# Kernel optimization log

Measured on AMD Instinct MI355X. Metric: run time of the kernel, lower is better.

Reference implementation:

```python
import jax, jax.numpy as jnp
import numpy as np

N = 50000       # nodes
E = 800000      # raw edges (self-loops added in reference, per PyG GATConv default)
F_IN = 256      # input feature dim (dataset.num_features stand-in)
H = 4           # heads (layer 1)
C = 32          # hidden_channels per head
CLS = 16        # num_classes (layer 2 out, heads=1)


def setup_inputs() -> dict:
    key = jax.random.key(0)
    ks = jax.random.split(key, 12)
    s = 0.05
    return {
        "x": jax.random.normal(ks[0], (N, F_IN), jnp.float32),
        "edge_index": jax.random.randint(ks[1], (2, E), 0, N, dtype=jnp.int64),
        "W1": jax.random.normal(ks[2], (F_IN, H * C), jnp.float32) * s,
        "att_src1": jax.random.normal(ks[3], (H, C), jnp.float32) * s,
        "att_dst1": jax.random.normal(ks[4], (H, C), jnp.float32) * s,
        "b1": jnp.zeros((H * C,), jnp.float32),
        "W2": jax.random.normal(ks[5], (H * C, CLS), jnp.float32) * s,
        "att_src2": jax.random.normal(ks[6], (1, CLS), jnp.float32) * s,
        "att_dst2": jax.random.normal(ks[7], (1, CLS), jnp.float32) * s,
        "b2": jnp.zeros((CLS,), jnp.float32),
    }


def gat_conv(x, src, dst, W, a_src, a_dst, b, heads, ch):
    """One GATConv (concat=True). src/dst include self-loops."""
    n = x.shape[0]
    h = (x @ W).reshape(n, heads, ch)                       # [N,H,C]
    alpha_s = jnp.sum(h * a_src, axis=-1)                   # [N,H]
    alpha_d = jnp.sum(h * a_dst, axis=-1)                   # [N,H]
    e = jax.nn.leaky_relu(alpha_s[src] + alpha_d[dst], 0.2) # [E',H]
    # segment softmax over incoming edges of each destination node
    m = jax.ops.segment_max(e, dst, num_segments=n)         # [N,H]
    ex = jnp.exp(e - m[dst])
    den = jax.ops.segment_sum(ex, dst, num_segments=n)      # [N,H]
    coef = ex / (den[dst] + 1e-16)                          # [E',H]
    # weighted scatter-aggregate of source features
    out = jax.ops.segment_sum(h[src] * coef[:, :, None], dst, num_segments=n)
    return out.reshape(n, heads * ch) + b


def reference(x, edge_index, W1, att_src1, att_dst1, b1, W2, att_src2, att_dst2, b2):
    n = x.shape[0]
    loop = jnp.arange(n, dtype=edge_index.dtype)
    src = jnp.concatenate([edge_index[0], loop])
    dst = jnp.concatenate([edge_index[1], loop])
    # eval mode: F.dropout is identity
    h = gat_conv(x, src, dst, W1, att_src1, att_dst1, b1, H, C)
    h = jax.nn.elu(h)
    out = gat_conv(h, src, dst, W2, att_src2, att_dst2, b2, 1, CLS)
    return out
```

## Files before the change

kernel.cpp:

```cpp
#include <hip/hip_runtime.h>
#include <hip/hip_bf16.h>
#include <math.h>

#define NNODES 50000
#define FIN 256
#define HH 4
#define CC 32
#define D1 128
#define CLS 16
#define NBUCK ((NNODES + 255) >> 8)
#define CHUNK 4096
#define GEMMBLK ((NNODES + 63) / 64)
#define WPREPBLK ((FIN*D1 + 255) / 256)

typedef __attribute__((ext_vector_type(8))) short bfrag8;
typedef __attribute__((ext_vector_type(4))) float facc4;

__device__ __forceinline__ float lrelu(float x){ return x > 0.f ? x : 0.2f*x; }

__device__ __forceinline__ float fexp(float x){
#if __has_builtin(__builtin_amdgcn_exp2f)
  return __builtin_amdgcn_exp2f(x * 1.4426950408889634f);
#else
  return exp2f(x * 1.4426950408889634f);
#endif
}

__device__ __forceinline__ unsigned short f2bu(float x){
  __hip_bfloat16 h = __float2bfloat16(x);
  return *reinterpret_cast<unsigned short*>(&h);
}
__device__ __forceinline__ unsigned int pbf(float a, float b){
  return (unsigned int)f2bu(a) | ((unsigned int)f2bu(b) << 16);
}
__device__ __forceinline__ float2 bf2x(unsigned int u){
  float2 r;
  r.x = __uint_as_float(u << 16);
  r.y = __uint_as_float(u & 0xffff0000u);
  return r;
}

__global__ __launch_bounds__(256) void k_count_wprep(
    const int* __restrict__ dsts, int* __restrict__ bcnt, int E, int nCnt,
    const float* __restrict__ W, unsigned short* __restrict__ Wt) {
  if ((int)blockIdx.x < nCnt) {
    __shared__ int cnt[NBUCK];
    for (int t=threadIdx.x; t<NBUCK; t+=256) cnt[t]=0;
    __syncthreads();
    int base = blockIdx.x*CHUNK, lim = min(base+CHUNK, E);
    for (int e = base+threadIdx.x; e < lim; e += 256)
      atomicAdd(&cnt[dsts[e]>>8], 1);
    __syncthreads();
    for (int t=threadIdx.x; t<NBUCK; t+=256)
      if (cnt[t]) atomicAdd(&bcnt[t], cnt[t]);
  } else {
    int t = ((int)blockIdx.x - nCnt)*256 + threadIdx.x;
    if (t < FIN*D1) {
      int k = t >> 7, c = t & 127;
      Wt[c*FIN + k] = f2bu(W[t]);
    }
  }
}

__global__ __launch_bounds__(256) void k_gemm1_scan(
    const float* __restrict__ x, const unsigned int* __restrict__ Wt,
    const float* __restrict__ asrc, const float* __restrict__ adst,
    unsigned int* __restrict__ h1b, float* __restrict__ as1, float* __restrict__ ad1,
    const int* __restrict__ bcnt, int* __restrict__ gstart, int* __restrict__ gcur) {
  __shared__ unsigned int Bs[128*256/2];
  __shared__ unsigned int As[64*64/2];
  if ((int)blockIdx.x >= GEMMBLK) {
    int t = threadIdx.x;
    int orig = (t < NBUCK) ? bcnt[t] : 0;
    int v = orig;
    int ln = t & 63, wv = t >> 6;
    #pragma unroll
    for (int off=1; off<64; off<<=1){ int u=__shfl_up(v,off,64); if(ln>=off) v+=u; }
    __shared__ int wsum[4], wbase[4];
    if (ln==63) wsum[wv]=v;
    __syncthreads();
    if (t==0){
      int s=0;
      for(int k=0;k<4;k++){ wbase[k]=s; s+=wsum[k]; }
    }
    __syncthreads();
    int incl = wbase[wv]+v;
    if (t < NBUCK){ gstart[t+1]=incl; gcur[t]=incl-orig; }
    if (t==0) gstart[0]=0;
    return;
  }
  int tid = threadIdx.x;
  int wv = tid >> 6, lane = tid & 63;
  int r0 = blockIdx.x * 64;

  for (int it = 0; it < 16; it++) {
    int w16 = it*256 + tid;
    int c = w16 >> 5, k8 = w16 & 31;
    uint4 v = ((const uint4*)Wt)[w16];
    int byt = (c*512 + k8*16) ^ ((c&7)<<4);
    *(uint4*)((char*)Bs + byt) = v;
  }

  facc4 acc[8];
  #pragma unroll
  for (int t=0;t<8;t++) acc[t] = (facc4){0.f,0.f,0.f,0.f};

  int arow = tid >> 2, apart = tid & 3;
  int mrow = lane & 15, kb = lane >> 4;

  for (int stage = 0; stage < 4; stage++) {
    int gr = r0 + arow;
    const float* src = x + (size_t)gr*FIN + stage*64 + apart*16;
    float4 f0, f1, f2, f3;
    if (gr < NNODES) {
      f0 = *(const float4*)(src);
      f1 = *(const float4*)(src+4);
      f2 = *(const float4*)(src+8);
      f3 = *(const float4*)(src+12);
    } else {
      f0 = f1 = f2 = f3 = make_float4(0.f,0.f,0.f,0.f);
    }
    uint4 u0, u1;
    u0.x = pbf(f0.x,f0.y); u0.y = pbf(f0.z,f0.w);
    u0.z = pbf(f1.x,f1.y); u0.w = pbf(f1.z,f1.w);
    u1.x = pbf(f2.x,f2.y); u1.y = pbf(f2.z,f2.w);
    u1.z = pbf(f3.x,f3.y); u1.w = pbf(f3.z,f3.w);
    __syncthreads();
    int b0 = (arow*128 + apart*32) ^ ((arow&7)<<4);
    int b1 = (arow*128 + apart*32 + 16) ^ ((arow&7)<<4);
    *(uint4*)((char*)As + b0) = u0;
    *(uint4*)((char*)As + b1) = u1;
    __syncthreads();
    #pragma unroll
    for (int ks = 0; ks < 2; ks++) {
      int row = wv*16 + mrow;
      int abyt = (row*128 + ks*64 + kb*16) ^ ((row&7)<<4);
      bfrag8 afrag = *(bfrag8*)((char*)As + abyt);
      #pragma unroll
      for (int ct = 0; ct < 8; ct++) {
        int c = ct*16 + mrow;
        int bbyt = (c*512 + stage*128 + ks*64 + kb*16) ^ ((c&7)<<4);
        bfrag8 bfrag = *(bfrag8*)((char*)Bs + bbyt);
        acc[ct] = __builtin_amdgcn_mfma_f32_16x16x32_bf16(afrag, bfrag, acc[ct], 0, 0, 0);
      }
    }
  }
  int orow0 = r0 + wv*16 + (lane>>4)*4;
  int ocol = lane & 15;
  float asr[8], adr[8];
  #pragma unroll
  for (int ct=0; ct<8; ct++){
    asr[ct] = asrc[ct*16 + ocol];
    adr[ct] = adst[ct*16 + ocol];
  }
  #pragma unroll
  for (int r=0; r<4; r++) {
    int gr = orow0 + r;
    float sh[4], dh[4];
    #pragma unroll
    for (int h=0; h<4; h++){
      sh[h] = acc[2*h][r]*asr[2*h] + acc[2*h+1][r]*asr[2*h+1];
      dh[h] = acc[2*h][r]*adr[2*h] + acc[2*h+1][r]*adr[2*h+1];
    }
    #pragma unroll
    for (int off=1; off<16; off<<=1){
      #pragma unroll
      for (int h=0;h<4;h++){
        sh[h] += __shfl_xor(sh[h], off, 64);
        dh[h] += __shfl_xor(dh[h], off, 64);
      }
    }
    if (gr < NNODES) {
      if (ocol == 0) {
        *(float4*)(as1 + (size_t)gr*4) = make_float4(sh[0], sh[1], sh[2], sh[3]);
        *(float4*)(ad1 + (size_t)gr*4) = make_float4(dh[0], dh[1], dh[2], dh[3]);
      }
      #pragma unroll
      for (int ct=0; ct<4; ct++)
        h1b[(size_t)gr*64 + ct*16 + ocol] = pbf(acc[ct][r], acc[ct+4][r]);
    }
  }
}

__global__ __launch_bounds__(256) void bin_kernel(const int* __restrict__ srcs,
                                                  const int* __restrict__ dsts,
                                                  int* __restrict__ gcur,
                                                  unsigned int* __restrict__ binned, int E) {
  __shared__ int cnt[NBUCK];
  __shared__ int rbase[NBUCK];
  for (int t=threadIdx.x; t<NBUCK; t+=256) cnt[t]=0;
  __syncthreads();
  int base = blockIdx.x*CHUNK, lim = min(base+CHUNK, E);
  for (int e = base+threadIdx.x; e < lim; e += 256)
    atomicAdd(&cnt[dsts[e]>>8], 1);
  __syncthreads();
  for (int t=threadIdx.x; t<NBUCK; t+=256){
    rbase[t] = cnt[t] ? atomicAdd(&gcur[t], cnt[t]) : 0;
    cnt[t] = 0;
  }
  __syncthreads();
  for (int e = base+threadIdx.x; e < lim; e += 256){
    int d = dsts[e], s = srcs[e];
    int b = d >> 8;
    int p = rbase[b] + atomicAdd(&cnt[b], 1);
    binned[p] = ((unsigned int)s << 8) | (unsigned int)(d & 255);
  }
}

__global__ __launch_bounds__(256) void bucketcsr_kernel(const int* __restrict__ gstart,
                                                        const unsigned int* __restrict__ binned,
                                                        int* __restrict__ offs,
                                                        unsigned short* __restrict__ srcsort, int E) {
  int b = blockIdx.x;
  int s0 = gstart[b], s1 = gstart[b+1];
  int t = threadIdx.x;
  __shared__ int cnt[256];
  __shared__ int cur[256];
  cnt[t] = 0;
  __syncthreads();
  for (int j = s0+t; j < s1; j += 256)
    atomicAdd(&cnt[binned[j] & 255], 1);
  __syncthreads();
  int orig = cnt[t], v = orig;
  int ln = t & 63, wv = t >> 6;
  #pragma unroll
  for (int off=1; off<64; off<<=1){ int u=__shfl_up(v,off,64); if(ln>=off) v+=u; }
  __shared__ int wsum[4], wbase[4];
  if (ln==63) wsum[wv]=v;
  __syncthreads();
  if (t==0){
    int s=0;
    for(int k=0;k<4;k++){ wbase[k]=s; s+=wsum[k]; }
  }
  __syncthreads();
  int excl = wbase[wv] + v - orig;
  cur[t] = excl;
  int node = b*256 + t;
  if (node < NNODES) offs[node] = s0 + excl;
  if (node == NNODES-1) offs[NNODES] = E;
  __syncthreads();
  for (int j = s0+t; j < s1; j += 256){
    unsigned int e = binned[j];
    int p = s0 + atomicAdd(&cur[e & 255], 1);
    srcsort[p] = (unsigned short)(e >> 8);
  }
}

__global__ __launch_bounds__(256) void agg1_kernel(
    const unsigned int* __restrict__ h1b, const float* __restrict__ as1,
    const float* __restrict__ ad1, const int* __restrict__ offs,
    const unsigned short* __restrict__ srcsort, const float* __restrict__ b1,
    unsigned int* __restrict__ out1p) {
  __shared__ float exs[4][4][64];
  __shared__ int   ss [4][64];
  int warp = threadIdx.x >> 6;
  int lane = threadIdx.x & 63;
  int i = blockIdx.x * 4 + warp;
  if (i >= NNODES) return;
  int start = offs[i], end = offs[i+1];
  float4 adv = *(const float4*)(ad1 + (size_t)i*4);
  float4 asv = *(const float4*)(as1 + (size_t)i*4);
  float ad[4] = {adv.x, adv.y, adv.z, adv.w};
  float wself[4];
  {
    float av[4] = {asv.x, asv.y, asv.z, asv.w};
    #pragma unroll
    for (int h=0;h<4;h++) wself[h] = fexp(lrelu(av[h] + ad[h]));
  }
  int hlo = lane >> 5, hhi = hlo + 2;
  float den[4] = {0.f, 0.f, 0.f, 0.f};
  float accA, accB;
  {
    float2 hv = bf2x(h1b[(size_t)i*64 + lane]);
    accA = wself[hlo] * hv.x; accB = wself[hhi] * hv.y;
  }
  for (int c0 = start; c0 < end; c0 += 64) {
    int cnt = min(64, end - c0);
    int j = c0 + lane;
    if (j < end) {
      int s = (int)srcsort[j];
      float4 a = *(const float4*)(as1 + (size_t)s*4);
      float e0 = fexp(lrelu(a.x + ad[0]));
      float e1 = fexp(lrelu(a.y + ad[1]));
      float e2 = fexp(lrelu(a.z + ad[2]));
      float e3 = fexp(lrelu(a.w + ad[3]));
      den[0] += e0; den[1] += e1; den[2] += e2; den[3] += e3;
      exs[warp][0][lane] = e0; exs[warp][1][lane] = e1;
      exs[warp][2][lane] = e2; exs[warp][3][lane] = e3;
      ss[warp][lane] = s;
    }
    #pragma unroll 8
    for (int j2 = 0; j2 < cnt; j2++) {
      int s = ss[warp][j2];
      float2 hv = bf2x(h1b[(size_t)s*64 + lane]);
      accA = fmaf(exs[warp][hlo][j2], hv.x, accA);
      accB = fmaf(exs[warp][hhi][j2], hv.y, accB);
    }
  }
  #pragma unroll
  for (int off=1; off<64; off<<=1) {
    #pragma unroll
    for (int h=0;h<4;h++) den[h] += __shfl_xor(den[h], off, 64);
  }
  float invlo = 1.f / (den[hlo] + wself[hlo] + 1e-16f);
  float invhi = 1.f / (den[hhi] + wself[hhi] + 1e-16f);
  float v0 = accA * invlo + b1[lane];
  float v1 = accB * invhi + b1[lane + 64];
  v0 = v0 > 0.f ? v0 : fexp(v0) - 1.f;
  v1 = v1 > 0.f ? v1 : fexp(v1) - 1.f;
  out1p[(size_t)i*64 + lane] = pbf(v0, v1);
}

__global__ __launch_bounds__(256) void layer2_proj_kernel(
    const unsigned int* __restrict__ out1p, const float* __restrict__ W2,
    const float* __restrict__ asrc2, const float* __restrict__ adst2,
    __hip_bfloat16* __restrict__ h2b, float* __restrict__ as2, float* __restrict__ ad2) {
  __shared__ float w_s[D1*CLS];
  for (int l = threadIdx.x; l < D1*CLS; l += 256) w_s[l] = W2[l];
  __syncthreads();
  int warp = threadIdx.x >> 6, lane = threadIdx.x & 63;
  int i = blockIdx.x*4 + warp;
  if (i >= NNODES) return;
  int c = lane & 15, kq = lane >> 4;
  const unsigned int* xp = out1p + (size_t)i*64 + (kq&1)*32;
  bool hi = kq >= 2;
  int kb = (kq&1)*32 + (hi ? 64 : 0);
  float acc = 0.f;
  #pragma unroll
  for (int q8=0; q8<8; q8++) {
    uint4 u = *(const uint4*)(xp + q8*4);
    float v0 = hi ? bf2x(u.x).y : bf2x(u.x).x;
    float v1 = hi ? bf2x(u.y).y : bf2x(u.y).x;
    float v2 = hi ? bf2x(u.z).y : bf2x(u.z).x;
    float v3 = hi ? bf2x(u.w).y : bf2x(u.w).x;
    int k = kb + q8*4;
    acc = fmaf(v0, w_s[(k+0)*CLS + c], acc);
    acc = fmaf(v1, w_s[(k+1)*CLS + c], acc);
    acc = fmaf(v2, w_s[(k+2)*CLS + c], acc);
    acc = fmaf(v3, w_s[(k+3)*CLS + c], acc);
  }
  acc += __shfl_xor(acc, 16, 64);
  acc += __shfl_xor(acc, 32, 64);
  if (lane < 16) h2b[(size_t)i*CLS + c] = __float2bfloat16(acc);
  float s = acc * asrc2[c];
  float d = acc * adst2[c];
  #pragma unroll
  for (int off=1; off<16; off<<=1) { s += __shfl_xor(s, off, 64); d += __shfl_xor(d, off, 64); }
  if (lane == 0) { as2[i] = s; ad2[i] = d; }
}

__global__ __launch_bounds__(256) void agg2_kernel(
    const unsigned int* __restrict__ h2b, const float* __restrict__ as2,
    const float* __restrict__ ad2, const int* __restrict__ offs,
    const unsigned short* __restrict__ srcsort, const float* __restrict__ b2,
    float* __restrict__ out) {
  int warp = threadIdx.x >> 6, lane = threadIdx.x & 63;
  int i = blockIdx.x*4 + warp;
  if (i >= NNODES) return;
  int start = offs[i], end = offs[i+1];
  float ad = ad2[i];
  float wself = fexp(lrelu(as2[i] + ad));
  int g = lane >> 3, cp = lane & 7;
  float2 acc = make_float2(0.f, 0.f);
  float denp = 0.f;
  if (g == 0) {
    float2 hv = bf2x(h2b[(size_t)i*(CLS/2) + cp]);
    acc.x = wself*hv.x; acc.y = wself*hv.y;
    denp = wself;
  }
  #pragma unroll 4
  for (int j = start + g; j < end; j += 8) {
    int s = (int)srcsort[j];
    float w = fexp(lrelu(as2[s] + ad));
    denp += w;
    float2 hv = bf2x(h2b[(size_t)s*(CLS/2) + cp]);
    acc.x = fmaf(w, hv.x, acc.x);
    acc.y = fmaf(w, hv.y, acc.y);
  }
  #pragma unroll
  for (int off=8; off<64; off<<=1) {
    acc.x += __shfl_xor(acc.x, off, 64);
    acc.y += __shfl_xor(acc.y, off, 64);
    denp  += __shfl_xor(denp,  off, 64);
  }
  if (lane < 8) {
    float inv = 1.f / (denp + 1e-16f);
    float2 o;
    o.x = acc.x * inv + b2[2*cp];
    o.y = acc.y * inv + b2[2*cp+1];
    *(float2*)(out + (size_t)i*CLS + 2*cp) = o;
  }
}

extern "C" void kernel_launch(void* const* d_in, const int* in_sizes, int n_in,
                              void* d_out, int out_size, void* d_ws, size_t ws_size,
                              hipStream_t stream) {
  const float* x     = (const float*)d_in[0];
  const int*   eidx  = (const int*)d_in[1];
  const float* W1    = (const float*)d_in[2];
  const float* asrc1 = (const float*)d_in[3];
  const float* adst1 = (const float*)d_in[4];
  const float* b1    = (const float*)d_in[5];
  const float* W2    = (const float*)d_in[6];
  const float* asrc2 = (const float*)d_in[7];
  const float* adst2 = (const float*)d_in[8];
  const float* b2    = (const float*)d_in[9];
  float* out = (float*)d_out;

  const int E = in_sizes[1] / 2;
  const int* srcs = eidx;
  const int* dsts = eidx + E;
  const int EBLK = (E + CHUNK - 1) / CHUNK;

  char* ws = (char*)d_ws;
  size_t off = 0;
  auto alloc = [&](size_t bytes) -> void* {
    void* p = ws + off;
    off = (off + bytes + 255) & ~(size_t)255;
    return p;
  };
  unsigned int*   h1b     = (unsigned int*)alloc((size_t)NNODES*(D1/2)*4);
  unsigned int*   out1p   = (unsigned int*)alloc((size_t)NNODES*(D1/2)*4);
  unsigned short* Wt      = (unsigned short*)alloc((size_t)FIN*D1*2);
  float*          as1     = (float*)alloc((size_t)NNODES*HH*4);
  float*          ad1     = (float*)alloc((size_t)NNODES*HH*4);
  __hip_bfloat16* h2b     = (__hip_bfloat16*)alloc((size_t)NNODES*CLS*2);
  float*          as2     = (float*)alloc((size_t)NNODES*4);
  float*          ad2     = (float*)alloc((size_t)NNODES*4);
  int*            bcnt    = (int*)alloc((size_t)NBUCK*4);
  int*            gstart  = (int*)alloc((size_t)(NBUCK+1)*4);
  int*            gcur    = (int*)alloc((size_t)NBUCK*4);
  int*            offs    = (int*)alloc((size_t)(NNODES+1)*4);
  unsigned int*   binned  = (unsigned int*)alloc((size_t)E*4);
  unsigned short* srcsort = (unsigned short*)alloc((size_t)E*2);

  (void)hipMemsetAsync(bcnt, 0, (size_t)NBUCK*4, stream);

  k_count_wprep<<<EBLK + WPREPBLK, 256, 0, stream>>>(dsts, bcnt, E, EBLK, W1, Wt);

  k_gemm1_scan<<<GEMMBLK + 1, 256, 0, stream>>>(x, (const unsigned int*)Wt,
                                                asrc1, adst1, h1b, as1, ad1,
                                                bcnt, gstart, gcur);

  bin_kernel<<<EBLK, 256, 0, stream>>>(srcs, dsts, gcur, binned, E);
  bucketcsr_kernel<<<NBUCK, 256, 0, stream>>>(gstart, binned, offs, srcsort, E);

  agg1_kernel<<<(NNODES+3)/4, 256, 0, stream>>>(h1b, as1, ad1, offs, srcsort, b1, out1p);

  layer2_proj_kernel<<<(NNODES+3)/4, 256, 0, stream>>>(out1p, W2, asrc2, adst2, h2b, as2, ad2);
  agg2_kernel<<<(NNODES+3)/4, 256, 0, stream>>>((const unsigned int*)h2b, as2, ad2, offs, srcsort, b2, out);
}
```

Baseline: 151.0 us.

## Fuse edge binning into GEMM launch and recompute bucket scan per block

The separate bin kernel is merged into the layer-1 GEMM launch as extra blocks placed ahead of the GEMM blocks. Each bin block and each bucketcsr block recomputes the bucket prefix scan locally from the bucket counts, so the global gstart/gcur arrays disappear and a zero-initialised progress counter takes their place. This removes one kernel launch and lets the memory-bound binning overlap with the compute-bound GEMM. In exchange every block repeats a small scan, and the large GEMM shared-memory footprint is also reserved for the bin blocks, which may limit their occupancy.

Result: faster. 143.3 us (-5.1%).

```diff
diff --git a/kernel.cpp b/kernel.cpp
--- a/kernel.cpp
+++ b/kernel.cpp
@@ -62,21 +62,26 @@
   }
 }
 
-__global__ __launch_bounds__(256) void k_gemm1_scan(
+__global__ __launch_bounds__(256) void k_bin_gemm(
     const float* __restrict__ x, const unsigned int* __restrict__ Wt,
     const float* __restrict__ asrc, const float* __restrict__ adst,
     unsigned int* __restrict__ h1b, float* __restrict__ as1, float* __restrict__ ad1,
-    const int* __restrict__ bcnt, int* __restrict__ gstart, int* __restrict__ gcur) {
+    const int* __restrict__ srcs, const int* __restrict__ dsts,
+    const int* __restrict__ bcnt, int* __restrict__ gprog,
+    unsigned int* __restrict__ binned, int E, int nBin) {
   __shared__ unsigned int Bs[128*256/2];
   __shared__ unsigned int As[64*64/2];
-  if ((int)blockIdx.x >= GEMMBLK) {
+  if ((int)blockIdx.x < nBin) {
+    __shared__ int cnt[NBUCK];
+    __shared__ int rbase[NBUCK];
+    __shared__ int gsh[NBUCK];
+    __shared__ int wsum[4], wbase[4];
     int t = threadIdx.x;
     int orig = (t < NBUCK) ? bcnt[t] : 0;
     int v = orig;
     int ln = t & 63, wv = t >> 6;
     #pragma unroll
     for (int off=1; off<64; off<<=1){ int u=__shfl_up(v,off,64); if(ln>=off) v+=u; }
-    __shared__ int wsum[4], wbase[4];
     if (ln==63) wsum[wv]=v;
     __syncthreads();
     if (t==0){
@@ -84,14 +89,29 @@
       for(int k=0;k<4;k++){ wbase[k]=s; s+=wsum[k]; }
     }
     __syncthreads();
-    int incl = wbase[wv]+v;
-    if (t < NBUCK){ gstart[t+1]=incl; gcur[t]=incl-orig; }
-    if (t==0) gstart[0]=0;
+    if (t < NBUCK) gsh[t] = wbase[wv] + v - orig;
+    for (int q=t; q<NBUCK; q+=256) cnt[q]=0;
+    __syncthreads();
+    int base = blockIdx.x*CHUNK, lim = min(base+CHUNK, E);
+    for (int e = base+t; e < lim; e += 256)
+      atomicAdd(&cnt[dsts[e]>>8], 1);
+    __syncthreads();
+    for (int q=t; q<NBUCK; q+=256){
+      rbase[q] = cnt[q] ? gsh[q] + atomicAdd(&gprog[q], cnt[q]) : 0;
+      cnt[q] = 0;
+    }
+    __syncthreads();
+    for (int e = base+t; e < lim; e += 256){
+      int d = dsts[e], s = srcs[e];
+      int b = d >> 8;
+      int p = rbase[b] + atomicAdd(&cnt[b], 1);
+      binned[p] = ((unsigned int)s << 8) | (unsigned int)(d & 255);
+    }
     return;
   }
   int tid = threadIdx.x;
   int wv = tid >> 6, lane = tid & 63;
-  int r0 = blockIdx.x * 64;
+  int r0 = ((int)blockIdx.x - nBin) * 64;
 
   for (int it = 0; it < 16; it++) {
     int w16 = it*256 + tid;
@@ -182,42 +202,35 @@
   }
 }
 
-__global__ __launch_bounds__(256) void bin_kernel(const int* __restrict__ srcs,
-                                                  const int* __restrict__ dsts,
-                                                  int* __restrict__ gcur,
-                                                  unsigned int* __restrict__ binned, int E) {
-  __shared__ int cnt[NBUCK];
-  __shared__ int rbase[NBUCK];
-  for (int t=threadIdx.x; t<NBUCK; t+=256) cnt[t]=0;
-  __syncthreads();
-  int base = blockIdx.x*CHUNK, lim = min(base+CHUNK, E);
-  for (int e = base+threadIdx.x; e < lim; e += 256)
-    atomicAdd(&cnt[dsts[e]>>8], 1);
-  __syncthreads();
-  for (int t=threadIdx.x; t<NBUCK; t+=256){
-    rbase[t] = cnt[t] ? atomicAdd(&gcur[t], cnt[t]) : 0;
-    cnt[t] = 0;
-  }
-  __syncthreads();
-  for (int e = base+threadIdx.x; e < lim; e += 256){
-    int d = dsts[e], s = srcs[e];
-    int b = d >> 8;
-    int p = rbase[b] + atomicAdd(&cnt[b], 1);
-    binned[p] = ((unsigned int)s << 8) | (unsigned int)(d & 255);
-  }
-}
-
-__global__ __launch_bounds__(256) void bucketcsr_kernel(const int* __restrict__ gstart,
+__global__ __launch_bounds__(256) void bucketcsr_kernel(const int* __restrict__ bcnt,
                                                         const unsigned int* __restrict__ binned,
                                                         int* __restrict__ offs,
                                                         unsigned short* __restrict__ srcsort, int E) {
   int b = blockIdx.x;
-  int s0 = gstart[b], s1 = gstart[b+1];
   int t = threadIdx.x;
+  __shared__ int gsh[NBUCK+1];
   __shared__ int cnt[256];
   __shared__ int cur[256];
+  __shared__ int wsum[4], wbase[4];
+  {
+    int orig = (t < NBUCK) ? bcnt[t] : 0;
+    int v = orig;
+    int ln = t & 63, wv = t >> 6;
+    #pragma unroll
+    for (int off=1; off<64; off<<=1){ int u=__shfl_up(v,off,64); if(ln>=off) v+=u; }
+    if (ln==63) wsum[wv]=v;
+    __syncthreads();
+    if (t==0){
+      int s=0;
+      for(int k=0;k<4;k++){ wbase[k]=s; s+=wsum[k]; }
+      gsh[0]=0;
+    }
+    __syncthreads();
+    if (t < NBUCK) gsh[t+1] = wbase[wv] + v;
+  }
   cnt[t] = 0;
   __syncthreads();
+  int s0 = gsh[b], s1 = gsh[b+1];
   for (int j = s0+t; j < s1; j += 256)
     atomicAdd(&cnt[binned[j] & 255], 1);
   __syncthreads();
@@ -225,7 +238,7 @@
   int ln = t & 63, wv = t >> 6;
   #pragma unroll
   for (int off=1; off<64; off<<=1){ int u=__shfl_up(v,off,64); if(ln>=off) v+=u; }
-  __shared__ int wsum[4], wbase[4];
+  __syncthreads();
   if (ln==63) wsum[wv]=v;
   __syncthreads();
   if (t==0){
@@ -427,23 +440,22 @@
   __hip_bfloat16* h2b     = (__hip_bfloat16*)alloc((size_t)NNODES*CLS*2);
   float*          as2     = (float*)alloc((size_t)NNODES*4);
   float*          ad2     = (float*)alloc((size_t)NNODES*4);
-  int*            bcnt    = (int*)alloc((size_t)NBUCK*4);
-  int*            gstart  = (int*)alloc((size_t)(NBUCK+1)*4);
-  int*            gcur    = (int*)alloc((size_t)NBUCK*4);
+  int*            bcnt    = (int*)alloc((size_t)NBUCK*2*4);
+  int*            gprog   = bcnt + NBUCK;
   int*            offs    = (int*)alloc((size_t)(NNODES+1)*4);
   unsigned int*   binned  = (unsigned int*)alloc((size_t)E*4);
   unsigned short* srcsort = (unsigned short*)alloc((size_t)E*2);
 
-  (void)hipMemsetAsync(bcnt, 0, (size_t)NBUCK*4, stream);
+  (void)hipMemsetAsync(bcnt, 0, (size_t)NBUCK*2*4, stream);
 
   k_count_wprep<<<EBLK + WPREPBLK, 256, 0, stream>>>(dsts, bcnt, E, EBLK, W1, Wt);
 
-  k_gemm1_scan<<<GEMMBLK + 1, 256, 0, stream>>>(x, (const unsigned int*)Wt,
-                                                asrc1, adst1, h1b, as1, ad1,
-                                                bcnt, gstart, gcur);
-
-  bin_kernel<<<EBLK, 256, 0, stream>>>(srcs, dsts, gcur, binned, E);
-  bucketcsr_kernel<<<NBUCK, 256, 0, stream>>>(gstart, binned, offs, srcsort, E);
+  k_bin_gemm<<<EBLK + GEMMBLK, 256, 0, stream>>>(x, (const unsigned int*)Wt,
+                                                 asrc1, adst1, h1b, as1, ad1,
+                                                 srcs, dsts, bcnt, gprog,
+                                                 binned, E, EBLK);
+
+  bucketcsr_kernel<<<NBUCK, 256, 0, stream>>>(bcnt, binned, offs, srcsort, E);
 
   agg1_kernel<<<(NNODES+3)/4, 256, 0, stream>>>(h1b, as1, ad1, offs, srcsort, b1, out1p);
 
```
